# Optimization experiments

Measured on AMD Instinct MI355X. Metric: run time of the kernel, lower is better.

The kernel has to match this reference:

```python
import jax, jax.numpy as jnp
import numpy as np

N_NODES = 40000
N_EDGES = 640000
D_FEAT = 128


def setup_inputs() -> dict:
    key = jax.random.key(0)
    k1, k2, k3, k4 = jax.random.split(key, 4)
    x = jax.random.normal(k1, (N_NODES, D_FEAT), dtype=jnp.float32)
    beta = jax.random.uniform(k2, (1,), dtype=jnp.float32)
    # random edges guaranteed to have NO self-loops (module removes them anyway)
    row = jax.random.randint(k3, (N_EDGES,), 0, N_NODES)
    col = (row + 1 + jax.random.randint(k4, (N_EDGES,), 0, N_NODES - 1)) % N_NODES
    edge_index = jnp.stack([row, col]).astype(jnp.int64)
    return {"x": x, "beta": beta, "edge_index": edge_index}


def reference(x, beta, edge_index):
    num_nodes = x.shape[0]
    row, col = edge_index[0], edge_index[1]
    # add_self_loops (remove_self_loops is a no-op: inputs have none)
    loop = jnp.arange(num_nodes, dtype=row.dtype)
    row = jnp.concatenate([row, loop])  # [E+N]
    col = jnp.concatenate([col, loop])
    # per-edge cosine similarity scaled by beta
    norm = jnp.linalg.norm(x, axis=1)  # [N]
    alpha = jnp.sum(x[row] * x[col], axis=1) / (norm[row] * norm[col])  # [E+N]
    alpha = alpha * beta[0]
    # segment softmax grouped by destination node (row)
    amax = jax.ops.segment_max(alpha, row, num_segments=num_nodes)  # [N]
    alpha = jnp.exp(alpha - amax[row])
    denom = jax.ops.segment_sum(alpha, row, num_segments=num_nodes)  # [N]
    alpha = alpha / denom[row]
    # spmm: weighted scatter-aggregate of neighbor features
    out = jax.ops.segment_sum(alpha[:, None] * x[col], row, num_segments=num_nodes)  # [N, F]
    return out
```

## Files before the change

### kernel.cpp

```cpp
#include <hip/hip_runtime.h>
#include <math.h>

#define N_NODES 40000
#define N_EDGES 640000
#define D_FEAT 128
#define SLOTS 48
#define GPN 4
#define MAXIT (SLOTS / GPN)

__global__ void build_kernel(const int4* __restrict__ rows4, const int4* __restrict__ cols4,
                             int* __restrict__ count, int* __restrict__ ell) {
    int i = blockIdx.x * blockDim.x + threadIdx.x;
    if (i < N_EDGES / 4) {
        int4 r4 = rows4[i];
        int4 c4 = cols4[i];
        int k;
        k = atomicAdd(&count[r4.x], 1); if (k < SLOTS) ell[r4.x * SLOTS + k] = c4.x;
        k = atomicAdd(&count[r4.y], 1); if (k < SLOTS) ell[r4.y * SLOTS + k] = c4.y;
        k = atomicAdd(&count[r4.z], 1); if (k < SLOTS) ell[r4.z * SLOTS + k] = c4.z;
        k = atomicAdd(&count[r4.w], 1); if (k < SLOTS) ell[r4.w * SLOTS + k] = c4.w;
    }
}

__global__ __launch_bounds__(256)
void fused_kernel(const float* __restrict__ x, const float* __restrict__ beta,
                  const int* __restrict__ count, const int* __restrict__ ell,
                  float* __restrict__ out) {
    __shared__ float red[4][2][GPN][132];
    const int wid  = threadIdx.x >> 6;
    const int lane = threadIdx.x & 63;
    const int h    = lane >> 5;
    const int l32  = lane & 31;
    const int g    = (lane >> 3) & 3;
    const int hl   = lane & 7;
    const int node = blockIdx.x * 8 + wid * 2 + h;
    const int deg  = min(count[node], SLOTS);
    const int NIT  = (deg + GPN - 1) >> 2;
    int mx = max(NIT, __shfl_xor(NIT, 32));
    const int* eb = ell + node * SLOTS;

    int cidx[MAXIT];
    #pragma unroll
    for (int j = 0; j < MAXIT; j++) {
        int p = j * GPN + g;
        cidx[j] = (p < deg) ? eb[p] : node;
    }

    const float* xrow = x + (size_t)node * D_FEAT;
    const float4* xn = (const float4*)xrow;
    float4 a0 = xn[hl], a1 = xn[8 + hl], a2 = xn[16 + hl], a3 = xn[24 + hl];
    float na2 = a0.x*a0.x + a0.y*a0.y + a0.z*a0.z + a0.w*a0.w
              + a1.x*a1.x + a1.y*a1.y + a1.z*a1.z + a1.w*a1.w
              + a2.x*a2.x + a2.y*a2.y + a2.z*a2.z + a2.w*a2.w
              + a3.x*a3.x + a3.y*a3.y + a3.z*a3.z + a3.w*a3.w;
    #pragma unroll
    for (int m = 1; m < 8; m <<= 1) na2 += __shfl_xor(na2, m);
    const float b0    = beta[0];
    const float scale = b0 * __frsqrt_rn(na2);
    const float selfw = __expf(b0);
    float4 acc0 = {0,0,0,0}, acc1 = {0,0,0,0}, acc2 = {0,0,0,0}, acc3 = {0,0,0,0};
    float den = 0.f;

    float4 A0, A1, A2, A3, B0, B1, B2, B3;
    {
        const float4* xc = (const float4*)(x + (size_t)cidx[0] * D_FEAT);
        A0 = xc[hl]; A1 = xc[8 + hl]; A2 = xc[16 + hl]; A3 = xc[24 + hl];
    }
    {
        const float4* xc = (const float4*)(x + (size_t)cidx[1] * D_FEAT);
        B0 = xc[hl]; B1 = xc[8 + hl]; B2 = xc[16 + hl]; B3 = xc[24 + hl];
    }

    #pragma unroll
    for (int j = 0; j < MAXIT; j++) {
        if (j >= mx) break;
        float dot = a0.x*A0.x + a0.y*A0.y + a0.z*A0.z + a0.w*A0.w
                  + a1.x*A1.x + a1.y*A1.y + a1.z*A1.z + a1.w*A1.w
                  + a2.x*A2.x + a2.y*A2.y + a2.z*A2.z + a2.w*A2.w
                  + a3.x*A3.x + a3.y*A3.y + a3.z*A3.z + a3.w*A3.w;
        float nb2 = A0.x*A0.x + A0.y*A0.y + A0.z*A0.z + A0.w*A0.w
                  + A1.x*A1.x + A1.y*A1.y + A1.z*A1.z + A1.w*A1.w
                  + A2.x*A2.x + A2.y*A2.y + A2.z*A2.z + A2.w*A2.w
                  + A3.x*A3.x + A3.y*A3.y + A3.z*A3.z + A3.w*A3.w;
        #pragma unroll
        for (int m = 1; m < 8; m <<= 1) {
            dot += __shfl_xor(dot, m);
            nb2 += __shfl_xor(nb2, m);
        }
        float w = (j * GPN + g < deg) ? __expf(dot * scale * __frsqrt_rn(nb2)) : 0.f;
        acc0.x += w*A0.x; acc0.y += w*A0.y; acc0.z += w*A0.z; acc0.w += w*A0.w;
        acc1.x += w*A1.x; acc1.y += w*A1.y; acc1.z += w*A1.z; acc1.w += w*A1.w;
        acc2.x += w*A2.x; acc2.y += w*A2.y; acc2.z += w*A2.z; acc2.w += w*A2.w;
        acc3.x += w*A3.x; acc3.y += w*A3.y; acc3.z += w*A3.z; acc3.w += w*A3.w;
        den += w;
        A0 = B0; A1 = B1; A2 = B2; A3 = B3;
        int cn = (j + 2 < MAXIT) ? cidx[j + 2] : node;
        const float4* xc = (const float4*)(x + (size_t)cn * D_FEAT);
        B0 = xc[hl]; B1 = xc[8 + hl]; B2 = xc[16 + hl]; B3 = xc[24 + hl];
    }

    den += __shfl_xor(den, 8);
    den += __shfl_xor(den, 16);

    {
        float4* rb = (float4*)red[wid][h][g];
        rb[      hl] = acc0;
        rb[ 8 + hl] = acc1;
        rb[16 + hl] = acc2;
        rb[24 + hl] = acc3;
    }
    float4 s = {0.f, 0.f, 0.f, 0.f};
    #pragma unroll
    for (int q = 0; q < GPN; q++) {
        float4 t = ((const float4*)red[wid][h][q])[l32];
        s.x += t.x; s.y += t.y; s.z += t.z; s.w += t.w;
    }
    float4 xs = ((const float4*)xrow)[l32];
    float inv = 1.0f / (den + selfw);
    float4 o = { (s.x + selfw * xs.x) * inv, (s.y + selfw * xs.y) * inv,
                 (s.z + selfw * xs.z) * inv, (s.w + selfw * xs.w) * inv };
    ((float4*)(out + (size_t)node * D_FEAT))[l32] = o;
}

extern "C" void kernel_launch(void* const* d_in, const int* in_sizes, int n_in,
                              void* d_out, int out_size, void* d_ws, size_t ws_size,
                              hipStream_t stream) {
    const float* x    = (const float*)d_in[0];
    const float* beta = (const float*)d_in[1];
    const int*   row  = (const int*)d_in[2];
    const int*   col  = row + N_EDGES;
    float*       out  = (float*)d_out;

    int* count = (int*)d_ws;
    int* ell   = count + N_NODES;

    hipMemsetAsync(count, 0, N_NODES * sizeof(int), stream);

    build_kernel<<<(N_EDGES / 4 + 255) / 256, 256, 0, stream>>>(
        (const int4*)row, (const int4*)col, count, ell);

    fused_kernel<<<N_NODES / 8, 256, 0, stream>>>(x, beta, count, ell, out);
}
```

Baseline: 89.52 us.

## Precompute inverse row norms and deepen gather prefetch to three stages

Adds a pre-pass kernel that zeroes the degree counters and computes each node's inverse L2 norm once. This replaces the memset and removes the per-edge norm computation and its shuffle reductions from the fused kernel. The fused kernel now loads one rinv value per neighbour and keeps three neighbour rows in flight instead of two. It also splits the dot product into two FMA chains, and the build kernel goes back to scalar one-edge-per-thread loads. The costs are an extra kernel launch that streams x once more and higher register pressure from the third prefetch buffer.

```diff
diff --git a/kernel.cpp b/kernel.cpp
--- a/kernel.cpp
+++ b/kernel.cpp
@@ -8,24 +8,36 @@
 #define GPN 4
 #define MAXIT (SLOTS / GPN)
 
-__global__ void build_kernel(const int4* __restrict__ rows4, const int4* __restrict__ cols4,
+#define FMA2(ax, ay, bx, by, w, cx, cy) { cx = fmaf(ax, bx, cx); cy = fmaf(ay, by, cy); (void)w; }
+
+__global__ void zero_rinv_kernel(const float* __restrict__ x, float* __restrict__ rinv,
+                                 int* __restrict__ count) {
+    int tid = blockIdx.x * blockDim.x + threadIdx.x;
+    if (tid < N_NODES) count[tid] = 0;
+    int node = tid >> 5;
+    int l    = tid & 31;
+    const float4* xp = (const float4*)(x + (size_t)node * D_FEAT);
+    float4 v = xp[l];
+    float s = v.x*v.x + v.y*v.y + v.z*v.z + v.w*v.w;
+    #pragma unroll
+    for (int m = 1; m < 32; m <<= 1) s += __shfl_xor(s, m);
+    if (l == 0) rinv[node] = __frsqrt_rn(s);
+}
+
+__global__ void build_kernel(const int* __restrict__ row, const int* __restrict__ col,
                              int* __restrict__ count, int* __restrict__ ell) {
     int i = blockIdx.x * blockDim.x + threadIdx.x;
-    if (i < N_EDGES / 4) {
-        int4 r4 = rows4[i];
-        int4 c4 = cols4[i];
-        int k;
-        k = atomicAdd(&count[r4.x], 1); if (k < SLOTS) ell[r4.x * SLOTS + k] = c4.x;
-        k = atomicAdd(&count[r4.y], 1); if (k < SLOTS) ell[r4.y * SLOTS + k] = c4.y;
-        k = atomicAdd(&count[r4.z], 1); if (k < SLOTS) ell[r4.z * SLOTS + k] = c4.z;
-        k = atomicAdd(&count[r4.w], 1); if (k < SLOTS) ell[r4.w * SLOTS + k] = c4.w;
+    if (i < N_EDGES) {
+        int r = row[i];
+        int rank = atomicAdd(&count[r], 1);
+        if (rank < SLOTS) ell[r * SLOTS + rank] = col[i];
     }
 }
 
 __global__ __launch_bounds__(256)
 void fused_kernel(const float* __restrict__ x, const float* __restrict__ beta,
-                  const int* __restrict__ count, const int* __restrict__ ell,
-                  float* __restrict__ out) {
+                  const float* __restrict__ rinv, const int* __restrict__ count,
+                  const int* __restrict__ ell, float* __restrict__ out) {
     __shared__ float red[4][2][GPN][132];
     const int wid  = threadIdx.x >> 6;
     const int lane = threadIdx.x & 63;
@@ -45,23 +57,20 @@
         int p = j * GPN + g;
         cidx[j] = (p < deg) ? eb[p] : node;
     }
+    float rv[MAXIT];
+    #pragma unroll
+    for (int j = 0; j < MAXIT; j++) rv[j] = rinv[cidx[j]];
 
     const float* xrow = x + (size_t)node * D_FEAT;
     const float4* xn = (const float4*)xrow;
     float4 a0 = xn[hl], a1 = xn[8 + hl], a2 = xn[16 + hl], a3 = xn[24 + hl];
-    float na2 = a0.x*a0.x + a0.y*a0.y + a0.z*a0.z + a0.w*a0.w
-              + a1.x*a1.x + a1.y*a1.y + a1.z*a1.z + a1.w*a1.w
-              + a2.x*a2.x + a2.y*a2.y + a2.z*a2.z + a2.w*a2.w
-              + a3.x*a3.x + a3.y*a3.y + a3.z*a3.z + a3.w*a3.w;
-    #pragma unroll
-    for (int m = 1; m < 8; m <<= 1) na2 += __shfl_xor(na2, m);
     const float b0    = beta[0];
-    const float scale = b0 * __frsqrt_rn(na2);
+    const float scale = b0 * rinv[node];
     const float selfw = __expf(b0);
     float4 acc0 = {0,0,0,0}, acc1 = {0,0,0,0}, acc2 = {0,0,0,0}, acc3 = {0,0,0,0};
     float den = 0.f;
 
-    float4 A0, A1, A2, A3, B0, B1, B2, B3;
+    float4 A0, A1, A2, A3, B0, B1, B2, B3, C0, C1, C2, C3;
     {
         const float4* xc = (const float4*)(x + (size_t)cidx[0] * D_FEAT);
         A0 = xc[hl]; A1 = xc[8 + hl]; A2 = xc[16 + hl]; A3 = xc[24 + hl];
@@ -70,33 +79,41 @@
         const float4* xc = (const float4*)(x + (size_t)cidx[1] * D_FEAT);
         B0 = xc[hl]; B1 = xc[8 + hl]; B2 = xc[16 + hl]; B3 = xc[24 + hl];
     }
+    {
+        const float4* xc = (const float4*)(x + (size_t)cidx[2] * D_FEAT);
+        C0 = xc[hl]; C1 = xc[8 + hl]; C2 = xc[16 + hl]; C3 = xc[24 + hl];
+    }
 
     #pragma unroll
     for (int j = 0; j < MAXIT; j++) {
         if (j >= mx) break;
-        float dot = a0.x*A0.x + a0.y*A0.y + a0.z*A0.z + a0.w*A0.w
-                  + a1.x*A1.x + a1.y*A1.y + a1.z*A1.z + a1.w*A1.w
-                  + a2.x*A2.x + a2.y*A2.y + a2.z*A2.z + a2.w*A2.w
-                  + a3.x*A3.x + a3.y*A3.y + a3.z*A3.z + a3.w*A3.w;
-        float nb2 = A0.x*A0.x + A0.y*A0.y + A0.z*A0.z + A0.w*A0.w
-                  + A1.x*A1.x + A1.y*A1.y + A1.z*A1.z + A1.w*A1.w
-                  + A2.x*A2.x + A2.y*A2.y + A2.z*A2.z + A2.w*A2.w
-                  + A3.x*A3.x + A3.y*A3.y + A3.z*A3.z + A3.w*A3.w;
+        float dx = 0.f, dy = 0.f;
+        FMA2(a0.x, a0.y, A0.x, A0.y, 0, dx, dy);
+        FMA2(a0.z, a0.w, A0.z, A0.w, 0, dx, dy);
+        FMA2(a1.x, a1.y, A1.x, A1.y, 0, dx, dy);
+        FMA2(a1.z, a1.w, A1.z, A1.w, 0, dx, dy);
+        FMA2(a2.x, a2.y, A2.x, A2.y, 0, dx, dy);
+        FMA2(a2.z, a2.w, A2.z, A2.w, 0, dx, dy);
+        FMA2(a3.x, a3.y, A3.x, A3.y, 0, dx, dy);
+        FMA2(a3.z, a3.w, A3.z, A3.w, 0, dx, dy);
+        float dot = dx + dy;
         #pragma unroll
-        for (int m = 1; m < 8; m <<= 1) {
-            dot += __shfl_xor(dot, m);
-            nb2 += __shfl_xor(nb2, m);
-        }
-        float w = (j * GPN + g < deg) ? __expf(dot * scale * __frsqrt_rn(nb2)) : 0.f;
-        acc0.x += w*A0.x; acc0.y += w*A0.y; acc0.z += w*A0.z; acc0.w += w*A0.w;
-        acc1.x += w*A1.x; acc1.y += w*A1.y; acc1.z += w*A1.z; acc1.w += w*A1.w;
-        acc2.x += w*A2.x; acc2.y += w*A2.y; acc2.z += w*A2.z; acc2.w += w*A2.w;
-        acc3.x += w*A3.x; acc3.y += w*A3.y; acc3.z += w*A3.z; acc3.w += w*A3.w;
+        for (int m = 1; m < 8; m <<= 1) dot += __shfl_xor(dot, m);
+        float w = (j * GPN + g < deg) ? __expf(dot * scale * rv[j]) : 0.f;
+        FMA2(A0.x, A0.y, w, w, 0, acc0.x, acc0.y);
+        FMA2(A0.z, A0.w, w, w, 0, acc0.z, acc0.w);
+        FMA2(A1.x, A1.y, w, w, 0, acc1.x, acc1.y);
+        FMA2(A1.z, A1.w, w, w, 0, acc1.z, acc1.w);
+        FMA2(A2.x, A2.y, w, w, 0, acc2.x, acc2.y);
+        FMA2(A2.z, A2.w, w, w, 0, acc2.z, acc2.w);
+        FMA2(A3.x, A3.y, w, w, 0, acc3.x, acc3.y);
+        FMA2(A3.z, A3.w, w, w, 0, acc3.z, acc3.w);
         den += w;
         A0 = B0; A1 = B1; A2 = B2; A3 = B3;
-        int cn = (j + 2 < MAXIT) ? cidx[j + 2] : node;
+        B0 = C0; B1 = C1; B2 = C2; B3 = C3;
+        int cn = (j + 3 < MAXIT) ? cidx[j + 3] : node;
         const float4* xc = (const float4*)(x + (size_t)cn * D_FEAT);
-        B0 = xc[hl]; B1 = xc[8 + hl]; B2 = xc[16 + hl]; B3 = xc[24 + hl];
+        C0 = xc[hl]; C1 = xc[8 + hl]; C2 = xc[16 + hl]; C3 = xc[24 + hl];
     }
 
     den += __shfl_xor(den, 8);
@@ -104,7 +121,7 @@
 
     {
         float4* rb = (float4*)red[wid][h][g];
-        rb[      hl] = acc0;
+        rb[     hl] = acc0;
         rb[ 8 + hl] = acc1;
         rb[16 + hl] = acc2;
         rb[24 + hl] = acc3;
@@ -131,13 +148,13 @@
     const int*   col  = row + N_EDGES;
     float*       out  = (float*)d_out;
 
-    int* count = (int*)d_ws;
-    int* ell   = count + N_NODES;
+    int*   count = (int*)d_ws;
+    float* rinv  = (float*)(count + N_NODES);
+    int*   ell   = (int*)(rinv + N_NODES);
 
-    hipMemsetAsync(count, 0, N_NODES * sizeof(int), stream);
+    zero_rinv_kernel<<<(N_NODES * 32) / 256, 256, 0, stream>>>(x, rinv, count);
 
-    build_kernel<<<(N_EDGES / 4 + 255) / 256, 256, 0, stream>>>(
-        (const int4*)row, (const int4*)col, count, ell);
+    build_kernel<<<(N_EDGES + 255) / 256, 256, 0, stream>>>(row, col, count, ell);
 
-    fused_kernel<<<N_NODES / 8, 256, 0, stream>>>(x, beta, count, ell, out);
+    fused_kernel<<<N_NODES / 8, 256, 0, stream>>>(x, beta, rinv, count, ell, out);
 }
```

After: 87.20 us. 1.03x faster.

## Process several nodes per warp with prefetched adjacency and deeper load pipeline

Applied to the files above, without the earlier changes.

The fused kernel now runs 1250 blocks and each half-wave handles four nodes in sequence. The next node's ELL adjacency list is prefetched while the current node is processed. The neighbor-row prefetch grows from two stages to three to hide more gather latency. The build kernel also moves from four edges per thread with int4 loads to one edge per thread. The trade-off is higher register pressure and fewer waves for the scheduler to hide latency with.

```diff
diff --git a/kernel.cpp b/kernel.cpp
--- a/kernel.cpp
+++ b/kernel.cpp
@@ -7,119 +7,147 @@
 #define SLOTS 48
 #define GPN 4
 #define MAXIT (SLOTS / GPN)
+#define BLOCKS 1250
+#define WPB 4
+#define PPW 4
 
-__global__ void build_kernel(const int4* __restrict__ rows4, const int4* __restrict__ cols4,
+__global__ void build_kernel(const int* __restrict__ row, const int* __restrict__ col,
                              int* __restrict__ count, int* __restrict__ ell) {
     int i = blockIdx.x * blockDim.x + threadIdx.x;
-    if (i < N_EDGES / 4) {
-        int4 r4 = rows4[i];
-        int4 c4 = cols4[i];
-        int k;
-        k = atomicAdd(&count[r4.x], 1); if (k < SLOTS) ell[r4.x * SLOTS + k] = c4.x;
-        k = atomicAdd(&count[r4.y], 1); if (k < SLOTS) ell[r4.y * SLOTS + k] = c4.y;
-        k = atomicAdd(&count[r4.z], 1); if (k < SLOTS) ell[r4.z * SLOTS + k] = c4.z;
-        k = atomicAdd(&count[r4.w], 1); if (k < SLOTS) ell[r4.w * SLOTS + k] = c4.w;
-    }
+    int r = row[i];
+    int rank = atomicAdd(&count[r], 1);
+    if (rank < SLOTS) ell[r * SLOTS + rank] = col[i];
 }
 
 __global__ __launch_bounds__(256)
 void fused_kernel(const float* __restrict__ x, const float* __restrict__ beta,
                   const int* __restrict__ count, const int* __restrict__ ell,
                   float* __restrict__ out) {
-    __shared__ float red[4][2][GPN][132];
+    __shared__ float red[WPB][2][GPN][132];
     const int wid  = threadIdx.x >> 6;
     const int lane = threadIdx.x & 63;
     const int h    = lane >> 5;
     const int l32  = lane & 31;
     const int g    = (lane >> 3) & 3;
     const int hl   = lane & 7;
-    const int node = blockIdx.x * 8 + wid * 2 + h;
-    const int deg  = min(count[node], SLOTS);
-    const int NIT  = (deg + GPN - 1) >> 2;
-    int mx = max(NIT, __shfl_xor(NIT, 32));
-    const int* eb = ell + node * SLOTS;
+    const int gw   = blockIdx.x * WPB + wid;
+    const float b0    = beta[0];
+    const float selfw = __expf(b0);
 
-    int cidx[MAXIT];
-    #pragma unroll
-    for (int j = 0; j < MAXIT; j++) {
-        int p = j * GPN + g;
-        cidx[j] = (p < deg) ? eb[p] : node;
+    const int nb = gw * (2 * PPW) + h;
+
+    int nxt[MAXIT]; int degn;
+    {
+        const int* eb = ell + nb * SLOTS;
+        degn = min(count[nb], SLOTS);
+        #pragma unroll
+        for (int j = 0; j < MAXIT; j++) {
+            int p = j * GPN + g;
+            nxt[j] = (p < degn) ? eb[p] : nb;
+        }
     }
 
-    const float* xrow = x + (size_t)node * D_FEAT;
-    const float4* xn = (const float4*)xrow;
-    float4 a0 = xn[hl], a1 = xn[8 + hl], a2 = xn[16 + hl], a3 = xn[24 + hl];
-    float na2 = a0.x*a0.x + a0.y*a0.y + a0.z*a0.z + a0.w*a0.w
-              + a1.x*a1.x + a1.y*a1.y + a1.z*a1.z + a1.w*a1.w
-              + a2.x*a2.x + a2.y*a2.y + a2.z*a2.z + a2.w*a2.w
-              + a3.x*a3.x + a3.y*a3.y + a3.z*a3.z + a3.w*a3.w;
-    #pragma unroll
-    for (int m = 1; m < 8; m <<= 1) na2 += __shfl_xor(na2, m);
-    const float b0    = beta[0];
-    const float scale = b0 * __frsqrt_rn(na2);
-    const float selfw = __expf(b0);
-    float4 acc0 = {0,0,0,0}, acc1 = {0,0,0,0}, acc2 = {0,0,0,0}, acc3 = {0,0,0,0};
-    float den = 0.f;
+    #pragma unroll 1
+    for (int k = 0; k < PPW; k++) {
+        const int node = nb + 2 * k;
+        const int deg  = degn;
+        int cidx[MAXIT];
+        #pragma unroll
+        for (int j = 0; j < MAXIT; j++) cidx[j] = nxt[j];
 
-    float4 A0, A1, A2, A3, B0, B1, B2, B3;
-    {
-        const float4* xc = (const float4*)(x + (size_t)cidx[0] * D_FEAT);
-        A0 = xc[hl]; A1 = xc[8 + hl]; A2 = xc[16 + hl]; A3 = xc[24 + hl];
+        if (k + 1 < PPW) {
+            const int nn = node + 2;
+            const int* eb = ell + nn * SLOTS;
+            degn = min(count[nn], SLOTS);
+            #pragma unroll
+            for (int j = 0; j < MAXIT; j++) {
+                int p = j * GPN + g;
+                nxt[j] = (p < degn) ? eb[p] : nn;
+            }
+        }
+
+        const int NIT = (deg + GPN - 1) >> 2;
+        const int mx  = max(NIT, __shfl_xor(NIT, 32));
+
+        const float* xrow = x + (size_t)node * D_FEAT;
+        const float4* xn  = (const float4*)xrow;
+        float4 a0 = xn[hl], a1 = xn[8 + hl], a2 = xn[16 + hl], a3 = xn[24 + hl];
+        float na2 = a0.x*a0.x + a0.y*a0.y + a0.z*a0.z + a0.w*a0.w
+                  + a1.x*a1.x + a1.y*a1.y + a1.z*a1.z + a1.w*a1.w
+                  + a2.x*a2.x + a2.y*a2.y + a2.z*a2.z + a2.w*a2.w
+                  + a3.x*a3.x + a3.y*a3.y + a3.z*a3.z + a3.w*a3.w;
+        #pragma unroll
+        for (int m = 1; m < 8; m <<= 1) na2 += __shfl_xor(na2, m);
+        const float scale = b0 * __frsqrt_rn(na2);
+
+        float4 acc0 = {0,0,0,0}, acc1 = {0,0,0,0}, acc2 = {0,0,0,0}, acc3 = {0,0,0,0};
+        float den = 0.f;
+
+        float4 A0, A1, A2, A3, B0, B1, B2, B3, C0, C1, C2, C3;
+        {
+            const float4* xc = (const float4*)(x + (size_t)cidx[0] * D_FEAT);
+            A0 = xc[hl]; A1 = xc[8 + hl]; A2 = xc[16 + hl]; A3 = xc[24 + hl];
+        }
+        {
+            const float4* xc = (const float4*)(x + (size_t)cidx[1] * D_FEAT);
+            B0 = xc[hl]; B1 = xc[8 + hl]; B2 = xc[16 + hl]; B3 = xc[24 + hl];
+        }
+        {
+            const float4* xc = (const float4*)(x + (size_t)cidx[2] * D_FEAT);
+            C0 = xc[hl]; C1 = xc[8 + hl]; C2 = xc[16 + hl]; C3 = xc[24 + hl];
+        }
+
+        #pragma unroll
+        for (int j = 0; j < MAXIT; j++) {
+            if (j >= mx) break;
+            float dot = a0.x*A0.x + a0.y*A0.y + a0.z*A0.z + a0.w*A0.w
+                      + a1.x*A1.x + a1.y*A1.y + a1.z*A1.z + a1.w*A1.w
+                      + a2.x*A2.x + a2.y*A2.y + a2.z*A2.z + a2.w*A2.w
+                      + a3.x*A3.x + a3.y*A3.y + a3.z*A3.z + a3.w*A3.w;
+            float nb2 = A0.x*A0.x + A0.y*A0.y + A0.z*A0.z + A0.w*A0.w
+                      + A1.x*A1.x + A1.y*A1.y + A1.z*A1.z + A1.w*A1.w
+                      + A2.x*A2.x + A2.y*A2.y + A2.z*A2.z + A2.w*A2.w
+                      + A3.x*A3.x + A3.y*A3.y + A3.z*A3.z + A3.w*A3.w;
+            #pragma unroll
+            for (int m = 1; m < 8; m <<= 1) {
+                dot += __shfl_xor(dot, m);
+                nb2 += __shfl_xor(nb2, m);
+            }
+            float w = (j * GPN + g < deg) ? __expf(dot * scale * __frsqrt_rn(nb2)) : 0.f;
+            acc0.x += w*A0.x; acc0.y += w*A0.y; acc0.z += w*A0.z; acc0.w += w*A0.w;
+            acc1.x += w*A1.x; acc1.y += w*A1.y; acc1.z += w*A1.z; acc1.w += w*A1.w;
+            acc2.x += w*A2.x; acc2.y += w*A2.y; acc2.z += w*A2.z; acc2.w += w*A2.w;
+            acc3.x += w*A3.x; acc3.y += w*A3.y; acc3.z += w*A3.z; acc3.w += w*A3.w;
+            den += w;
+            A0 = B0; A1 = B1; A2 = B2; A3 = B3;
+            B0 = C0; B1 = C1; B2 = C2; B3 = C3;
+            int cn = (j + 3 < MAXIT) ? cidx[j + 3] : node;
+            const float4* xc = (const float4*)(x + (size_t)cn * D_FEAT);
+            C0 = xc[hl]; C1 = xc[8 + hl]; C2 = xc[16 + hl]; C3 = xc[24 + hl];
+        }
+
+        den += __shfl_xor(den, 8);
+        den += __shfl_xor(den, 16);
+
+        {
+            float4* rb = (float4*)red[wid][h][g];
+            rb[     hl] = acc0;
+            rb[ 8 + hl] = acc1;
+            rb[16 + hl] = acc2;
+            rb[24 + hl] = acc3;
+        }
+        float4 s = {0.f, 0.f, 0.f, 0.f};
+        #pragma unroll
+        for (int q = 0; q < GPN; q++) {
+            float4 t = ((const float4*)red[wid][h][q])[l32];
+            s.x += t.x; s.y += t.y; s.z += t.z; s.w += t.w;
+        }
+        float4 xs = ((const float4*)xrow)[l32];
+        float inv = 1.0f / (den + selfw);
+        float4 o = { (s.x + selfw * xs.x) * inv, (s.y + selfw * xs.y) * inv,
+                     (s.z + selfw * xs.z) * inv, (s.w + selfw * xs.w) * inv };
+        ((float4*)(out + (size_t)node * D_FEAT))[l32] = o;
     }
-    {
-        const float4* xc = (const float4*)(x + (size_t)cidx[1] * D_FEAT);
-        B0 = xc[hl]; B1 = xc[8 + hl]; B2 = xc[16 + hl]; B3 = xc[24 + hl];
-    }
-
-    #pragma unroll
-    for (int j = 0; j < MAXIT; j++) {
-        if (j >= mx) break;
-        float dot = a0.x*A0.x + a0.y*A0.y + a0.z*A0.z + a0.w*A0.w
-                  + a1.x*A1.x + a1.y*A1.y + a1.z*A1.z + a1.w*A1.w
-                  + a2.x*A2.x + a2.y*A2.y + a2.z*A2.z + a2.w*A2.w
-                  + a3.x*A3.x + a3.y*A3.y + a3.z*A3.z + a3.w*A3.w;
-        float nb2 = A0.x*A0.x + A0.y*A0.y + A0.z*A0.z + A0.w*A0.w
-                  + A1.x*A1.x + A1.y*A1.y + A1.z*A1.z + A1.w*A1.w
-                  + A2.x*A2.x + A2.y*A2.y + A2.z*A2.z + A2.w*A2.w
-                  + A3.x*A3.x + A3.y*A3.y + A3.z*A3.z + A3.w*A3.w;
-        #pragma unroll
-        for (int m = 1; m < 8; m <<= 1) {
-            dot += __shfl_xor(dot, m);
-            nb2 += __shfl_xor(nb2, m);
-        }
-        float w = (j * GPN + g < deg) ? __expf(dot * scale * __frsqrt_rn(nb2)) : 0.f;
-        acc0.x += w*A0.x; acc0.y += w*A0.y; acc0.z += w*A0.z; acc0.w += w*A0.w;
-        acc1.x += w*A1.x; acc1.y += w*A1.y; acc1.z += w*A1.z; acc1.w += w*A1.w;
-        acc2.x += w*A2.x; acc2.y += w*A2.y; acc2.z += w*A2.z; acc2.w += w*A2.w;
-        acc3.x += w*A3.x; acc3.y += w*A3.y; acc3.z += w*A3.z; acc3.w += w*A3.w;
-        den += w;
-        A0 = B0; A1 = B1; A2 = B2; A3 = B3;
-        int cn = (j + 2 < MAXIT) ? cidx[j + 2] : node;
-        const float4* xc = (const float4*)(x + (size_t)cn * D_FEAT);
-        B0 = xc[hl]; B1 = xc[8 + hl]; B2 = xc[16 + hl]; B3 = xc[24 + hl];
-    }
-
-    den += __shfl_xor(den, 8);
-    den += __shfl_xor(den, 16);
-
-    {
-        float4* rb = (float4*)red[wid][h][g];
-        rb[      hl] = acc0;
-        rb[ 8 + hl] = acc1;
-        rb[16 + hl] = acc2;
-        rb[24 + hl] = acc3;
-    }
-    float4 s = {0.f, 0.f, 0.f, 0.f};
-    #pragma unroll
-    for (int q = 0; q < GPN; q++) {
-        float4 t = ((const float4*)red[wid][h][q])[l32];
-        s.x += t.x; s.y += t.y; s.z += t.z; s.w += t.w;
-    }
-    float4 xs = ((const float4*)xrow)[l32];
-    float inv = 1.0f / (den + selfw);
-    float4 o = { (s.x + selfw * xs.x) * inv, (s.y + selfw * xs.y) * inv,
-                 (s.z + selfw * xs.z) * inv, (s.w + selfw * xs.w) * inv };
-    ((float4*)(out + (size_t)node * D_FEAT))[l32] = o;
 }
 
 extern "C" void kernel_launch(void* const* d_in, const int* in_sizes, int n_in,
@@ -136,8 +164,7 @@
 
     hipMemsetAsync(count, 0, N_NODES * sizeof(int), stream);
 
-    build_kernel<<<(N_EDGES / 4 + 255) / 256, 256, 0, stream>>>(
-        (const int4*)row, (const int4*)col, count, ell);
+    build_kernel<<<N_EDGES / 256, 256, 0, stream>>>(row, col, count, ell);
 
-    fused_kernel<<<N_NODES / 8, 256, 0, stream>>>(x, beta, count, ell, out);
+    fused_kernel<<<BLOCKS, 256, 0, stream>>>(x, beta, count, ell, out);
 }
```

Result: slower. 97.72 us (+9.2%).
